# Performance work log

Hardware: AMD Instinct MI355X
Metric: run time of the kernel (lower is better)

The kernel has to match this reference:

```python
import jax, jax.numpy as jnp
import numpy as np

N, M, D = 8192, 8192, 64


def setup_inputs() -> dict:
    key = jax.random.key(0)
    kx, ky = jax.random.split(key)
    X = jax.random.normal(kx, (N, D), dtype=jnp.float32)
    Y = jax.random.normal(ky, (M, D), dtype=jnp.float32)
    return {"X": X, "Y": Y}


def reference(X, Y):
    # Pairwise Euclidean distances via the |x|^2 + |y|^2 - 2<x,y> identity
    # (avoids materializing the [N, M, D] difference tensor).
    x2 = jnp.sum(X * X, axis=1)[:, None]          # [N, 1]
    y2 = jnp.sum(Y * Y, axis=1)[None, :]          # [1, M]
    d2 = x2 + y2 - 2.0 * (X @ Y.T)                # [N, M]
    d = jnp.sqrt(jnp.maximum(d2, 0.0))            # Euclidean distance matrix
    dis_1 = jnp.mean(jnp.min(d, axis=1))          # avg over X of nearest-in-Y
    dis_2 = jnp.mean(jnp.min(d, axis=0))          # avg over Y of nearest-in-X
    return dis_1 + dis_2
```

## Files before the change

### kernel.cpp

```cpp
#include <hip/hip_runtime.h>
#include <math.h>


#define NROWS 8192
#define DDIM  64
#define ITILES 64
#define SLICES 8
#define CHUNKS 8
#define LSTR 72

typedef __bf16 bf16_t;
typedef bf16_t bf16x8 __attribute__((ext_vector_type(8)));
typedef float  f32x4  __attribute__((ext_vector_type(4)));

__global__ void prep_kernel(const float* __restrict__ X,
                            const float* __restrict__ Y,
                            bf16_t* __restrict__ Xbf, bf16_t* __restrict__ Ybf,
                            float* __restrict__ x2, float* __restrict__ y2,
                            float* __restrict__ out) {
  int t = blockIdx.x * blockDim.x + threadIdx.x;
  int half = t >> 15;
  int r = (t >> 2) & (NROWS - 1);
  int part = t & 3;
  const float* src = half ? Y : X;
  bf16_t* dst = half ? Ybf : Xbf;
  float* sq = half ? y2 : x2;
  const float scale = half ? 1.0f : -2.0f;

  const float4* p = (const float4*)(src + r * DDIM + part * 16);
  float4 v0 = p[0], v1 = p[1], v2 = p[2], v3 = p[3];
  float s = 0.f;
  s = fmaf(v0.x, v0.x, s); s = fmaf(v0.y, v0.y, s);
  s = fmaf(v0.z, v0.z, s); s = fmaf(v0.w, v0.w, s);
  s = fmaf(v1.x, v1.x, s); s = fmaf(v1.y, v1.y, s);
  s = fmaf(v1.z, v1.z, s); s = fmaf(v1.w, v1.w, s);
  s = fmaf(v2.x, v2.x, s); s = fmaf(v2.y, v2.y, s);
  s = fmaf(v2.z, v2.z, s); s = fmaf(v2.w, v2.w, s);
  s = fmaf(v3.x, v3.x, s); s = fmaf(v3.y, v3.y, s);
  s = fmaf(v3.z, v3.z, s); s = fmaf(v3.w, v3.w, s);

  bf16x8 h0 = {(bf16_t)(scale * v0.x), (bf16_t)(scale * v0.y),
               (bf16_t)(scale * v0.z), (bf16_t)(scale * v0.w),
               (bf16_t)(scale * v1.x), (bf16_t)(scale * v1.y),
               (bf16_t)(scale * v1.z), (bf16_t)(scale * v1.w)};
  bf16x8 h1 = {(bf16_t)(scale * v2.x), (bf16_t)(scale * v2.y),
               (bf16_t)(scale * v2.z), (bf16_t)(scale * v2.w),
               (bf16_t)(scale * v3.x), (bf16_t)(scale * v3.y),
               (bf16_t)(scale * v3.z), (bf16_t)(scale * v3.w)};
  *(bf16x8*)&dst[r * DDIM + part * 16] = h0;
  *(bf16x8*)&dst[r * DDIM + part * 16 + 8] = h1;

  s += __shfl_xor(s, 1, 64);
  s += __shfl_xor(s, 2, 64);
  if (part == 0) sq[r] = s;
  if (t == 0) out[0] = 0.f;
}

__global__ __launch_bounds__(256, 2)
void mine_kernel(const bf16_t* __restrict__ Xbf, const bf16_t* __restrict__ Ybf,
                 const float* __restrict__ x2g, const float* __restrict__ y2g,
                 float* __restrict__ rslab, float* __restrict__ cslab) {
  __shared__ bf16_t Ys[2][128 * LSTR];
  __shared__ float credL[2][2][128];

  const int tid = threadIdx.x;
  const int L = tid & 63;
  const int w = tid >> 6;
  const int lr = L & 15;
  const int q = L >> 4;
  const int rh = w >> 1;
  const int ch = w & 1;
  const int itile = blockIdx.x & (ITILES - 1);
  const int slice = blockIdx.x >> 6;
  const int i0 = itile * 128;
  const int rgb = rh * 64;
  const int cgb = ch * 64;
  const int jbase = slice * (CHUNKS * 128);

  bf16x8 Af[8];
#pragma unroll
  for (int a = 0; a < 4; ++a) {
    int row = i0 + rgb + a * 16 + lr;
#pragma unroll
    for (int h = 0; h < 2; ++h)
      Af[a * 2 + h] = *(const bf16x8*)&Xbf[row * DDIM + h * 32 + q * 8];
  }
  float x2r[16];
#pragma unroll
  for (int a = 0; a < 4; ++a) {
    float4 v = *(const float4*)&x2g[i0 + rgb + a * 16 + q * 4];
    x2r[a * 4 + 0] = v.x; x2r[a * 4 + 1] = v.y;
    x2r[a * 4 + 2] = v.z; x2r[a * 4 + 3] = v.w;
  }

  float rmin[16];
#pragma unroll
  for (int k = 0; k < 16; ++k) rmin[k] = INFINITY;

  bf16x8 Bst[4];
#pragma unroll
  for (int p = 0; p < 4; ++p) {
    int f = p * 256 + tid;
    Bst[p] = *(const bf16x8*)&Ybf[(jbase + (f >> 3)) * DDIM + (f & 7) * 8];
  }
#pragma unroll
  for (int p = 0; p < 4; ++p) {
    int f = p * 256 + tid;
    *(bf16x8*)&Ys[0][(f >> 3) * LSTR + (f & 7) * 8] = Bst[p];
  }
  __syncthreads();

  for (int cc = 0; cc < CHUNKS; ++cc) {
    const bf16_t* Yb = Ys[cc & 1];

    float y2c[4];
#pragma unroll
    for (int b = 0; b < 4; ++b)
      y2c[b] = y2g[jbase + cc * 128 + cgb + b * 16 + lr];

    if (cc + 1 < CHUNKS) {
      int j0n = jbase + (cc + 1) * 128;
#pragma unroll
      for (int p = 0; p < 4; ++p) {
        int f = p * 256 + tid;
        Bst[p] = *(const bf16x8*)&Ybf[(j0n + (f >> 3)) * DDIM + (f & 7) * 8];
      }
    }

    f32x4 acc[4][4];
#pragma unroll
    for (int a = 0; a < 4; ++a)
#pragma unroll
      for (int b = 0; b < 4; ++b) {
        acc[a][b][0] = x2r[a * 4 + 0] + y2c[b];
        acc[a][b][1] = x2r[a * 4 + 1] + y2c[b];
        acc[a][b][2] = x2r[a * 4 + 2] + y2c[b];
        acc[a][b][3] = x2r[a * 4 + 3] + y2c[b];
      }

#pragma unroll
    for (int b = 0; b < 4; ++b) {
      bf16x8 B0 = *(const bf16x8*)&Yb[(cgb + b * 16 + lr) * LSTR + q * 8];
      bf16x8 B1 = *(const bf16x8*)&Yb[(cgb + b * 16 + lr) * LSTR + 32 + q * 8];
#pragma unroll
      for (int a = 0; a < 4; ++a) {
        acc[a][b] = __builtin_amdgcn_mfma_f32_16x16x32_bf16(Af[a * 2 + 0], B0, acc[a][b], 0, 0, 0);
        acc[a][b] = __builtin_amdgcn_mfma_f32_16x16x32_bf16(Af[a * 2 + 1], B1, acc[a][b], 0, 0, 0);
      }
    }

    float cmin[4] = {INFINITY, INFINITY, INFINITY, INFINITY};
#pragma unroll
    for (int a = 0; a < 4; ++a) {
#pragma unroll
      for (int p = 0; p < 4; ++p) {
        float rm = rmin[a * 4 + p];
        rm = fminf(fminf(rm, acc[a][0][p]), acc[a][1][p]);
        rmin[a * 4 + p] = fminf(fminf(rm, acc[a][2][p]), acc[a][3][p]);
      }
#pragma unroll
      for (int b = 0; b < 4; ++b) {
        float cm = cmin[b];
        cm = fminf(fminf(cm, acc[a][b][0]), acc[a][b][1]);
        cmin[b] = fminf(fminf(cm, acc[a][b][2]), acc[a][b][3]);
      }
    }
#pragma unroll
    for (int b = 0; b < 4; ++b) {
      cmin[b] = fminf(cmin[b], __shfl_xor(cmin[b], 16, 64));
      cmin[b] = fminf(cmin[b], __shfl_xor(cmin[b], 32, 64));
    }
    float v = cmin[0];
    if (q == 1) v = cmin[1];
    else if (q == 2) v = cmin[2];
    else if (q == 3) v = cmin[3];
    credL[cc & 1][rh][cgb + L] = v;

    if (cc + 1 < CHUNKS) {
      bf16_t* Yn = Ys[(cc + 1) & 1];
#pragma unroll
      for (int p = 0; p < 4; ++p) {
        int f = p * 256 + tid;
        *(bf16x8*)&Yn[(f >> 3) * LSTR + (f & 7) * 8] = Bst[p];
      }
    }
    __syncthreads();

    if (tid < 128) {
      float m = fminf(credL[cc & 1][0][tid], credL[cc & 1][1][tid]);
      cslab[itile * NROWS + jbase + cc * 128 + tid] = m;
    }
  }

#pragma unroll
  for (int a = 0; a < 4; ++a)
#pragma unroll
    for (int p = 0; p < 4; ++p) {
      float v = rmin[a * 4 + p];
      v = fminf(v, __shfl_xor(v, 1, 64));
      v = fminf(v, __shfl_xor(v, 2, 64));
      v = fminf(v, __shfl_xor(v, 4, 64));
      v = fminf(v, __shfl_xor(v, 8, 64));
      if (lr == 0)
        rslab[slice * (NROWS * 2) + (i0 + rgb + a * 16 + q * 4 + p) * 2 + ch] = v;
    }
}

__global__ void finish_kernel(const float* __restrict__ rslab,
                              const float* __restrict__ cslab,
                              float* __restrict__ out) {
  const int b = blockIdx.x;
  const int tid = threadIdx.x;
  if (b < 32) {
    int row = b * 256 + tid;
    float m = INFINITY;
#pragma unroll
    for (int g = 0; g < SLICES; ++g) {
      float2 v = *(const float2*)&rslab[g * (NROWS * 2) + row * 2];
      m = fminf(m, fminf(v.x, v.y));
    }
    float v = sqrtf(fmaxf(m, 0.f)) * (1.0f / 8192.0f);
#pragma unroll
    for (int off = 32; off > 0; off >>= 1) v += __shfl_down(v, off, 64);
    __shared__ float partial[4];
    if ((tid & 63) == 0) partial[tid >> 6] = v;
    __syncthreads();
    if (tid == 0)
      atomicAdd(out, partial[0] + partial[1] + partial[2] + partial[3]);
  } else {
    int j = (b - 32) * 64 + (tid & 63);
    int seg = tid >> 6;
    float m = INFINITY;
#pragma unroll
    for (int k = 0; k < 16; ++k)
      m = fminf(m, cslab[(seg * 16 + k) * NROWS + j]);
    __shared__ float red[4][64];
    red[seg][tid & 63] = m;
    __syncthreads();
    if (tid < 64) {
      float mc = fminf(fminf(red[0][tid], red[1][tid]),
                       fminf(red[2][tid], red[3][tid]));
      float v = sqrtf(fmaxf(mc, 0.f)) * (1.0f / 8192.0f);
#pragma unroll
      for (int off = 32; off > 0; off >>= 1) v += __shfl_down(v, off, 64);
      if (tid == 0) atomicAdd(out, v);
    }
  }
}

extern "C" void kernel_launch(void* const* d_in, const int* in_sizes, int n_in,
                              void* d_out, int out_size, void* d_ws, size_t ws_size,
                              hipStream_t stream) {
  const float* X = (const float*)d_in[0];
  const float* Y = (const float*)d_in[1];
  float* out = (float*)d_out;

  char* wsb = (char*)d_ws;
  bf16_t* Xbf = (bf16_t*)wsb;
  bf16_t* Ybf = (bf16_t*)(wsb + (size_t)NROWS * DDIM * 2);
  float* x2 = (float*)(wsb + 2 * (size_t)NROWS * DDIM * 2);
  float* y2 = x2 + NROWS;
  float* rslab = y2 + NROWS;
  float* cslab = rslab + SLICES * NROWS * 2;

  prep_kernel<<<(2 * NROWS * 4) / 256, 256, 0, stream>>>(X, Y, Xbf, Ybf, x2, y2, out);
  mine_kernel<<<ITILES * SLICES, 256, 0, stream>>>(Xbf, Ybf, x2, y2, rslab, cslab);
  finish_kernel<<<160, 256, 0, stream>>>(rslab, cslab, out);
}
```

Before: 78.86 us.

## Fuse bf16 conversion and squared-norm prep into the main distance kernel

Result: slower. 86.01 us (+9.1%).

```diff
diff --git a/kernel.cpp b/kernel.cpp
--- a/kernel.cpp
+++ b/kernel.cpp
@@ -13,54 +13,13 @@
 typedef bf16_t bf16x8 __attribute__((ext_vector_type(8)));
 typedef float  f32x4  __attribute__((ext_vector_type(4)));
 
-__global__ void prep_kernel(const float* __restrict__ X,
-                            const float* __restrict__ Y,
-                            bf16_t* __restrict__ Xbf, bf16_t* __restrict__ Ybf,
-                            float* __restrict__ x2, float* __restrict__ y2,
-                            float* __restrict__ out) {
-  int t = blockIdx.x * blockDim.x + threadIdx.x;
-  int half = t >> 15;
-  int r = (t >> 2) & (NROWS - 1);
-  int part = t & 3;
-  const float* src = half ? Y : X;
-  bf16_t* dst = half ? Ybf : Xbf;
-  float* sq = half ? y2 : x2;
-  const float scale = half ? 1.0f : -2.0f;
-
-  const float4* p = (const float4*)(src + r * DDIM + part * 16);
-  float4 v0 = p[0], v1 = p[1], v2 = p[2], v3 = p[3];
-  float s = 0.f;
-  s = fmaf(v0.x, v0.x, s); s = fmaf(v0.y, v0.y, s);
-  s = fmaf(v0.z, v0.z, s); s = fmaf(v0.w, v0.w, s);
-  s = fmaf(v1.x, v1.x, s); s = fmaf(v1.y, v1.y, s);
-  s = fmaf(v1.z, v1.z, s); s = fmaf(v1.w, v1.w, s);
-  s = fmaf(v2.x, v2.x, s); s = fmaf(v2.y, v2.y, s);
-  s = fmaf(v2.z, v2.z, s); s = fmaf(v2.w, v2.w, s);
-  s = fmaf(v3.x, v3.x, s); s = fmaf(v3.y, v3.y, s);
-  s = fmaf(v3.z, v3.z, s); s = fmaf(v3.w, v3.w, s);
-
-  bf16x8 h0 = {(bf16_t)(scale * v0.x), (bf16_t)(scale * v0.y),
-               (bf16_t)(scale * v0.z), (bf16_t)(scale * v0.w),
-               (bf16_t)(scale * v1.x), (bf16_t)(scale * v1.y),
-               (bf16_t)(scale * v1.z), (bf16_t)(scale * v1.w)};
-  bf16x8 h1 = {(bf16_t)(scale * v2.x), (bf16_t)(scale * v2.y),
-               (bf16_t)(scale * v2.z), (bf16_t)(scale * v2.w),
-               (bf16_t)(scale * v3.x), (bf16_t)(scale * v3.y),
-               (bf16_t)(scale * v3.z), (bf16_t)(scale * v3.w)};
-  *(bf16x8*)&dst[r * DDIM + part * 16] = h0;
-  *(bf16x8*)&dst[r * DDIM + part * 16 + 8] = h1;
-
-  s += __shfl_xor(s, 1, 64);
-  s += __shfl_xor(s, 2, 64);
-  if (part == 0) sq[r] = s;
-  if (t == 0) out[0] = 0.f;
-}
-
 __global__ __launch_bounds__(256, 2)
-void mine_kernel(const bf16_t* __restrict__ Xbf, const bf16_t* __restrict__ Ybf,
-                 const float* __restrict__ x2g, const float* __restrict__ y2g,
-                 float* __restrict__ rslab, float* __restrict__ cslab) {
+void mine_kernel(const float* __restrict__ X, const float* __restrict__ Y,
+                 float* __restrict__ rslab, float* __restrict__ cslab,
+                 float* __restrict__ out) {
   __shared__ bf16_t Ys[2][128 * LSTR];
+  __shared__ float y2L[2][128];
+  __shared__ float x2s[128];
   __shared__ float credL[2][2][128];
 
   const int tid = threadIdx.x;
@@ -77,18 +36,63 @@
   const int cgb = ch * 64;
   const int jbase = slice * (CHUNKS * 128);
 
+  if (blockIdx.x == 0 && tid == 0) out[0] = 0.f;
+
+  {
+    int r = tid >> 1, hh = tid & 1;
+    const float4* xp = (const float4*)(X + (i0 + r) * DDIM + hh * 32);
+    float s = 0.f;
+#pragma unroll
+    for (int k = 0; k < 8; ++k) {
+      float4 v = xp[k];
+      s = fmaf(v.x, v.x, s); s = fmaf(v.y, v.y, s);
+      s = fmaf(v.z, v.z, s); s = fmaf(v.w, v.w, s);
+    }
+    s += __shfl_xor(s, 1, 64);
+    if (hh == 0) x2s[r] = s;
+  }
+
   bf16x8 Af[8];
 #pragma unroll
   for (int a = 0; a < 4; ++a) {
     int row = i0 + rgb + a * 16 + lr;
 #pragma unroll
-    for (int h = 0; h < 2; ++h)
-      Af[a * 2 + h] = *(const bf16x8*)&Xbf[row * DDIM + h * 32 + q * 8];
-  }
+    for (int h = 0; h < 2; ++h) {
+      const float4* xp = (const float4*)(X + row * DDIM + h * 32 + q * 8);
+      float4 u0 = xp[0], u1 = xp[1];
+      Af[a * 2 + h] = (bf16x8){
+          (bf16_t)(-2.f * u0.x), (bf16_t)(-2.f * u0.y),
+          (bf16_t)(-2.f * u0.z), (bf16_t)(-2.f * u0.w),
+          (bf16_t)(-2.f * u1.x), (bf16_t)(-2.f * u1.y),
+          (bf16_t)(-2.f * u1.z), (bf16_t)(-2.f * u1.w)};
+    }
+  }
+
+#pragma unroll
+  for (int p = 0; p < 4; ++p) {
+    int f = p * 256 + tid;
+    int row = f >> 3, part = f & 7;
+    const float4* yp = (const float4*)(Y + (jbase + row) * DDIM + part * 8);
+    float4 u0 = yp[0], u1 = yp[1];
+    float s = 0.f;
+    s = fmaf(u0.x, u0.x, s); s = fmaf(u0.y, u0.y, s);
+    s = fmaf(u0.z, u0.z, s); s = fmaf(u0.w, u0.w, s);
+    s = fmaf(u1.x, u1.x, s); s = fmaf(u1.y, u1.y, s);
+    s = fmaf(u1.z, u1.z, s); s = fmaf(u1.w, u1.w, s);
+    bf16x8 hv = {(bf16_t)u0.x, (bf16_t)u0.y, (bf16_t)u0.z, (bf16_t)u0.w,
+                 (bf16_t)u1.x, (bf16_t)u1.y, (bf16_t)u1.z, (bf16_t)u1.w};
+    *(bf16x8*)&Ys[0][row * LSTR + part * 8] = hv;
+    s += __shfl_xor(s, 1, 64);
+    s += __shfl_xor(s, 2, 64);
+    s += __shfl_xor(s, 4, 64);
+    if (part == 0) y2L[0][row] = s;
+  }
+  __syncthreads();
+
   float x2r[16];
 #pragma unroll
   for (int a = 0; a < 4; ++a) {
-    float4 v = *(const float4*)&x2g[i0 + rgb + a * 16 + q * 4];
+    float4 v = *(const float4*)&x2s[rgb + a * 16 + q * 4];
     x2r[a * 4 + 0] = v.x; x2r[a * 4 + 1] = v.y;
     x2r[a * 4 + 2] = v.z; x2r[a * 4 + 3] = v.w;
   }
@@ -97,18 +101,7 @@
 #pragma unroll
   for (int k = 0; k < 16; ++k) rmin[k] = INFINITY;
 
-  bf16x8 Bst[4];
-#pragma unroll
-  for (int p = 0; p < 4; ++p) {
-    int f = p * 256 + tid;
-    Bst[p] = *(const bf16x8*)&Ybf[(jbase + (f >> 3)) * DDIM + (f & 7) * 8];
-  }
-#pragma unroll
-  for (int p = 0; p < 4; ++p) {
-    int f = p * 256 + tid;
-    *(bf16x8*)&Ys[0][(f >> 3) * LSTR + (f & 7) * 8] = Bst[p];
-  }
-  __syncthreads();
+  float4 Nst[8];
 
   for (int cc = 0; cc < CHUNKS; ++cc) {
     const bf16_t* Yb = Ys[cc & 1];
@@ -116,14 +109,17 @@
     float y2c[4];
 #pragma unroll
     for (int b = 0; b < 4; ++b)
-      y2c[b] = y2g[jbase + cc * 128 + cgb + b * 16 + lr];
+      y2c[b] = y2L[cc & 1][cgb + b * 16 + lr];
 
     if (cc + 1 < CHUNKS) {
       int j0n = jbase + (cc + 1) * 128;
 #pragma unroll
       for (int p = 0; p < 4; ++p) {
         int f = p * 256 + tid;
-        Bst[p] = *(const bf16x8*)&Ybf[(j0n + (f >> 3)) * DDIM + (f & 7) * 8];
+        int row = f >> 3, part = f & 7;
+        const float4* yp = (const float4*)(Y + (j0n + row) * DDIM + part * 8);
+        Nst[p * 2] = yp[0];
+        Nst[p * 2 + 1] = yp[1];
       }
     }
 
@@ -178,10 +174,24 @@
 
     if (cc + 1 < CHUNKS) {
       bf16_t* Yn = Ys[(cc + 1) & 1];
+      float* y2n = y2L[(cc + 1) & 1];
 #pragma unroll
       for (int p = 0; p < 4; ++p) {
         int f = p * 256 + tid;
-        *(bf16x8*)&Yn[(f >> 3) * LSTR + (f & 7) * 8] = Bst[p];
+        int row = f >> 3, part = f & 7;
+        float4 u0 = Nst[p * 2], u1 = Nst[p * 2 + 1];
+        float s = 0.f;
+        s = fmaf(u0.x, u0.x, s); s = fmaf(u0.y, u0.y, s);
+        s = fmaf(u0.z, u0.z, s); s = fmaf(u0.w, u0.w, s);
+        s = fmaf(u1.x, u1.x, s); s = fmaf(u1.y, u1.y, s);
+        s = fmaf(u1.z, u1.z, s); s = fmaf(u1.w, u1.w, s);
+        bf16x8 hv = {(bf16_t)u0.x, (bf16_t)u0.y, (bf16_t)u0.z, (bf16_t)u0.w,
+                     (bf16_t)u1.x, (bf16_t)u1.y, (bf16_t)u1.z, (bf16_t)u1.w};
+        *(bf16x8*)&Yn[row * LSTR + part * 8] = hv;
+        s += __shfl_xor(s, 1, 64);
+        s += __shfl_xor(s, 2, 64);
+        s += __shfl_xor(s, 4, 64);
+        if (part == 0) y2n[row] = s;
       }
     }
     __syncthreads();
@@ -256,14 +266,9 @@
   float* out = (float*)d_out;
 
   char* wsb = (char*)d_ws;
-  bf16_t* Xbf = (bf16_t*)wsb;
-  bf16_t* Ybf = (bf16_t*)(wsb + (size_t)NROWS * DDIM * 2);
-  float* x2 = (float*)(wsb + 2 * (size_t)NROWS * DDIM * 2);
-  float* y2 = x2 + NROWS;
-  float* rslab = y2 + NROWS;
+  float* rslab = (float*)wsb;
   float* cslab = rslab + SLICES * NROWS * 2;
 
-  prep_kernel<<<(2 * NROWS * 4) / 256, 256, 0, stream>>>(X, Y, Xbf, Ybf, x2, y2, out);
-  mine_kernel<<<ITILES * SLICES, 256, 0, stream>>>(Xbf, Ybf, x2, y2, rslab, cslab);
+  mine_kernel<<<ITILES * SLICES, 256, 0, stream>>>(X, Y, rslab, cslab, out);
   finish_kernel<<<160, 256, 0, stream>>>(rslab, cslab, out);
 }
```
